# Kernel optimization log

Measured on AMD Instinct MI355X. Metric: run time of the kernel, lower is better.

Reference implementation:

```python
import jax, jax.numpy as jnp
import numpy as np

E = 768   # embed_size
H = 64    # head_embed_size
B = 8
T = 4096  # == ctx_size


def setup_inputs() -> dict:
    key = jax.random.key(0)
    k1, k2, k3, k4 = jax.random.split(key, 4)
    inputs = jax.random.normal(k1, (B, T, E), dtype=jnp.float32)
    # Linear weights stored as (E, H) so projection is x @ W
    scale = 1.0 / np.sqrt(E)
    Wq = jax.random.uniform(k2, (E, H), dtype=jnp.float32, minval=-scale, maxval=scale)
    Wk = jax.random.uniform(k3, (E, H), dtype=jnp.float32, minval=-scale, maxval=scale)
    Wv = jax.random.uniform(k4, (E, H), dtype=jnp.float32, minval=-scale, maxval=scale)
    return {"inputs": inputs, "Wq": Wq, "Wk": Wk, "Wv": Wv}


def reference(inputs, Wq, Wk, Wv):
    Tlen = inputs.shape[1]
    q = inputs @ Wq  # (B,T,H)
    k = inputs @ Wk  # (B,T,H)
    v = inputs @ Wv  # (B,T,H)
    # NOTE: original module does NOT scale by 1/sqrt(H) — faithful reproduction.
    scores = jnp.einsum('bqh,bkh->bqk', q, k)  # (B,T,T)
    causal = jnp.tril(jnp.ones((Tlen, Tlen), dtype=bool))
    scores = jnp.where(causal, scores, -jnp.inf)
    attn = jax.nn.softmax(scores, axis=-1)
    # dropout=0 -> identity
    out = jnp.einsum('bqk,bkh->bqh', attn, v)  # (B,T,H)
    return out
```

## Files before the change

### kernel.cpp

```cpp
#include <hip/hip_runtime.h>
#include <hip/hip_bf16.h>

#define E_DIM 768
#define H_DIM 64
#define B_SZ 8
#define T_SZ 4096
#define BT (B_SZ * T_SZ)

typedef __attribute__((ext_vector_type(8))) short short8;
typedef __attribute__((ext_vector_type(4))) float floatx4;

#define RAWBAR() __asm__ volatile("s_waitcnt lgkmcnt(0)\n\ts_barrier" ::: "memory")

static __device__ __forceinline__ unsigned short bf1(float a) {
    __hip_bfloat16 h = __float2bfloat16(a);
    unsigned short u; __builtin_memcpy(&u, &h, 2); return u;
}
static __device__ __forceinline__ unsigned int pk2(float a, float b) {
    __hip_bfloat162 h = __float22bfloat162_rn(float2{a, b});
    unsigned int u; __builtin_memcpy(&u, &h, 4); return u;
}

__global__ __launch_bounds__(256) void prep_w(
    const float* __restrict__ Wq, const float* __restrict__ Wk,
    const float* __restrict__ Wv, unsigned short* __restrict__ Wt)
{
    __shared__ float Ls[64][65];
    const int nt = blockIdx.x;
    const int kc = blockIdx.y;
    const float* __restrict__ W = (nt == 0) ? Wq : (nt == 1) ? Wk : Wv;
    const int t = threadIdx.x;
    const int k0 = kc * 64;

#pragma unroll
    for (int it = 0; it < 16; ++it) {
        const int kk = (t >> 6) + it * 4;
        Ls[kk][t & 63] = W[(size_t)(k0 + kk) * H_DIM + (t & 63)];
    }
    __syncthreads();

#pragma unroll
    for (int it = 0; it < 4; ++it) {
        const int nl = (t >> 4) + it * 16;
        const int kl = (t & 15) * 4;
        unsigned int u[2];
        u[0] = pk2(Ls[kl + 0][nl], Ls[kl + 1][nl]);
        u[1] = pk2(Ls[kl + 2][nl], Ls[kl + 3][nl]);
        *(uint2*)(Wt + (size_t)(nt * 64 + nl) * E_DIM + k0 + kl) = *(uint2*)u;
    }
}

__global__ __launch_bounds__(768) void proj_mfma(
    const float* __restrict__ X, const unsigned short* __restrict__ Wt,
    unsigned short* __restrict__ Qb, unsigned short* __restrict__ Kb,
    unsigned short* __restrict__ Vtb)
{
    __shared__ unsigned short Xs[2][16][776];

    const int tid  = threadIdx.x;
    const int wave = tid >> 6, lane = tid & 63;
    const int row  = lane & 15, quad = lane >> 4;
    const int m0   = blockIdx.x * 128;

    short8 bfr[24];
    {
        const unsigned short* wp = Wt + (size_t)(wave * 16 + row) * E_DIM + quad * 8;
#pragma unroll
        for (int ks = 0; ks < 24; ++ks) bfr[ks] = *(const short8*)(wp + ks * 32);
    }

    const int srow = tid & 15;
    const int sc   = tid >> 4;
    const float* __restrict__ xbase = X + (size_t)(m0 + srow) * E_DIM + sc * 16;

    float4 fx[4];
#define LDX(mt)                                                               \
    {                                                                         \
        const float* p = xbase + (size_t)(mt) * 16 * E_DIM;                   \
        fx[0] = *(const float4*)(p);     fx[1] = *(const float4*)(p + 4);     \
        fx[2] = *(const float4*)(p + 8); fx[3] = *(const float4*)(p + 12);    \
    }
#define STX(buf)                                                              \
    {                                                                         \
        unsigned int tmp[8];                                                  \
        tmp[0] = pk2(fx[0].x, fx[0].y); tmp[1] = pk2(fx[0].z, fx[0].w);       \
        tmp[2] = pk2(fx[1].x, fx[1].y); tmp[3] = pk2(fx[1].z, fx[1].w);       \
        tmp[4] = pk2(fx[2].x, fx[2].y); tmp[5] = pk2(fx[2].z, fx[2].w);       \
        tmp[6] = pk2(fx[3].x, fx[3].y); tmp[7] = pk2(fx[3].z, fx[3].w);       \
        *(int4*)&Xs[buf][srow][sc * 16]     = *(int4*)&tmp[0];                \
        *(int4*)&Xs[buf][srow][sc * 16 + 8] = *(int4*)&tmp[4];                \
    }

    LDX(0); STX(0);
    RAWBAR();

    const int g  = wave >> 2;
    const int h  = (wave & 3) * 16 + row;
    unsigned short* __restrict__ OQK = (g == 0) ? Qb : Kb;
    const int bb = m0 >> 12;

    int cur = 0;
    for (int mt = 0; mt < 8; ++mt) {
        if (mt < 7) LDX(mt + 1);

        floatx4 acc = (floatx4)0.0f;
#pragma unroll
        for (int ks = 0; ks < 24; ++ks) {
            const short8 af = *(const short8*)&Xs[cur][row][ks * 32 + quad * 8];
            acc = __builtin_amdgcn_mfma_f32_16x16x32_bf16(af, bfr[ks], acc, 0, 0, 0);
        }

        const int mr = m0 + mt * 16 + quad * 4;
        if (g < 2) {
#pragma unroll
            for (int r = 0; r < 4; ++r)
                OQK[(size_t)(mr + r) * H_DIM + h] = bf1(acc[r]);
        } else {
            const int t0 = mr & 4095;
            unsigned int u[2];
            u[0] = pk2(acc[0], acc[1]); u[1] = pk2(acc[2], acc[3]);
            *(uint2*)(Vtb + ((size_t)bb * H_DIM + h) * T_SZ + t0) = *(uint2*)u;
        }

        if (mt < 7) STX(cur ^ 1);
        RAWBAR();
        cur ^= 1;
    }
#undef LDX
#undef STX
}

typedef unsigned short KVrow[72];

__global__ __launch_bounds__(256) void attn_mfma(
    const unsigned short* __restrict__ Qb,
    const unsigned short* __restrict__ Kb,
    const unsigned short* __restrict__ Vtb,
    float* __restrict__ Out)
{
    __shared__ unsigned short Ks[3][64][72];
    __shared__ unsigned short Vs[3][64][72];
    __shared__ unsigned short Ps[4][16][76];

    const int lb   = blockIdx.x;
    const int b    = lb & 7;
    const int qt   = 63 - (lb >> 3);
    const int tid  = threadIdx.x;
    const int wave = tid >> 6, lane = tid & 63;
    const int row  = lane & 15, quad = lane >> 4;

    const size_t base = (size_t)b * T_SZ * H_DIM;
    const int q0 = qt * 64 + wave * 16;

    const int krow = tid >> 2, kcol = (tid & 3) * 16;
    const unsigned short* __restrict__ Ksrc = Kb + base + (size_t)krow * H_DIM + kcol;
    const int vh = tid >> 2, vseg = (tid & 3) * 16;
    const unsigned short* __restrict__ Vsrc = Vtb + ((size_t)b * H_DIM + vh) * T_SZ + vseg;

    short8 qf0, qf1;
    {
        const unsigned short* qp = Qb + base + (size_t)(q0 + row) * H_DIM + quad * 8;
        qf0 = *(const short8*)(qp);
        qf1 = *(const short8*)(qp + 32);
    }

    floatx4 o[4];
#pragma unroll
    for (int i = 0; i < 4; ++i) o[i] = (floatx4)0.0f;
    float lp[4] = {0.0f, 0.0f, 0.0f, 0.0f};

    KVrow* kp0 = Ks[0]; KVrow* kp1 = Ks[1]; KVrow* kp2 = Ks[2];
    KVrow* vp0 = Vs[0]; KVrow* vp1 = Vs[1]; KVrow* vp2 = Vs[2];

    int4 kA0, kA1, vA0, vA1, kB0, kB1, vB0, vB1;

#define LDKV(K0, K1, V0, V1, t)                                          \
    {                                                                    \
        const unsigned short* kp = Ksrc + (size_t)(t) * 64 * H_DIM;      \
        K0 = *(const int4*)kp; K1 = *(const int4*)(kp + 8);              \
        const unsigned short* vp = Vsrc + (t) * 64;                      \
        V0 = *(const int4*)vp; V1 = *(const int4*)(vp + 8);              \
    }
#define STKV(K0, K1, V0, V1, KD, VD)                                     \
    {                                                                    \
        *(int4*)&KD[krow][kcol] = K0; *(int4*)&KD[krow][kcol + 8] = K1;  \
        *(int4*)&VD[vh][vseg]   = V0; *(int4*)&VD[vh][vseg + 8]   = V1;  \
    }
#define ROTATE()                                                         \
    { KVrow* tk = kp0; kp0 = kp1; kp1 = kp2; kp2 = tk;                   \
      KVrow* tv = vp0; vp0 = vp1; vp1 = vp2; vp2 = tv; }

    auto compute = [&](int t, KVrow* kc, KVrow* vc) {
        floatx4 s[4];
#pragma unroll
        for (int nt = 0; nt < 4; ++nt) {
            const unsigned short* kp = &kc[nt * 16 + row][quad * 8];
            floatx4 a = (floatx4)0.0f;
            a = __builtin_amdgcn_mfma_f32_16x16x32_bf16(qf0, *(const short8*)(kp),      a, 0, 0, 0);
            a = __builtin_amdgcn_mfma_f32_16x16x32_bf16(qf1, *(const short8*)(kp + 32), a, 0, 0, 0);
            s[nt] = a;
        }
        if (t == qt) {
#pragma unroll
            for (int nt = 0; nt < 4; ++nt) {
                const int key_loc = nt * 16 + row;
#pragma unroll
                for (int r = 0; r < 4; ++r)
                    if (key_loc > wave * 16 + quad * 4 + r) s[nt][r] = -1e30f;
            }
        }
#pragma unroll
        for (int r = 0; r < 4; ++r) {
#pragma unroll
            for (int nt = 0; nt < 4; ++nt) {
                const float pv = __expf(fminf(s[nt][r], 80.0f));
                lp[r] += pv;
                Ps[wave][quad * 4 + r][nt * 16 + row] = bf1(pv);
            }
        }
        __builtin_amdgcn_wave_barrier();
#pragma unroll
        for (int kst = 0; kst < 2; ++kst) {
            const short8 pa = *(const short8*)(&Ps[wave][row][kst * 32 + quad * 8]);
#pragma unroll
            for (int nt = 0; nt < 4; ++nt) {
                const short8 vb = *(const short8*)(&vc[nt * 16 + row][kst * 32 + quad * 8]);
                o[nt] = __builtin_amdgcn_mfma_f32_16x16x32_bf16(pa, vb, o[nt], 0, 0, 0);
            }
        }
    };

    LDKV(kA0, kA1, vA0, vA1, 0);
    STKV(kA0, kA1, vA0, vA1, kp0, vp0);
    if (qt >= 1) LDKV(kB0, kB1, vB0, vB1, 1);
    RAWBAR();

    int kt = 0;
    while (true) {
        if (kt + 2 <= qt) LDKV(kA0, kA1, vA0, vA1, kt + 2);
        if (kt + 1 <= qt) STKV(kB0, kB1, vB0, vB1, kp1, vp1);
        compute(kt, kp0, vp0);
        RAWBAR();
        ROTATE();
        ++kt;
        if (kt > qt) break;

        if (kt + 2 <= qt) LDKV(kB0, kB1, vB0, vB1, kt + 2);
        if (kt + 1 <= qt) STKV(kA0, kA1, vA0, vA1, kp1, vp1);
        compute(kt, kp0, vp0);
        RAWBAR();
        ROTATE();
        ++kt;
        if (kt > qt) break;
    }

#pragma unroll
    for (int r = 0; r < 4; ++r) {
        float l = lp[r];
#pragma unroll
        for (int off = 1; off < 16; off <<= 1)
            l += __shfl_xor(l, off, 16);
        const float inv = 1.0f / l;
        float* op = Out + base + (size_t)(q0 + quad * 4 + r) * H_DIM + row;
#pragma unroll
        for (int nt = 0; nt < 4; ++nt)
            op[nt * 16] = o[nt][r] * inv;
    }
#undef LDKV
#undef STKV
#undef ROTATE
}

extern "C" void kernel_launch(void* const* d_in, const int* in_sizes, int n_in,
                              void* d_out, int out_size, void* d_ws, size_t ws_size,
                              hipStream_t stream) {
    const float* X  = (const float*)d_in[0];
    const float* Wq = (const float*)d_in[1];
    const float* Wk = (const float*)d_in[2];
    const float* Wv = (const float*)d_in[3];

    unsigned short* Wt  = (unsigned short*)d_ws;
    unsigned short* Qb  = Wt + (size_t)192 * E_DIM;
    unsigned short* Kb  = Qb + (size_t)BT * H_DIM;
    unsigned short* Vtb = Kb + (size_t)BT * H_DIM;

    prep_w<<<dim3(3, 12), 256, 0, stream>>>(Wq, Wk, Wv, Wt);
    proj_mfma<<<256, 768, 0, stream>>>(X, Wt, Qb, Kb, Vtb);
    attn_mfma<<<512, 256, 0, stream>>>(Qb, Kb, Vtb, (float*)d_out);
}
```

Measured before the change: 237.9 us.

## Split attention key range across waves with 16-row query blocks and LDS reduction

The attention kernel now assigns 16 query rows per block and splits the causal key tiles across the four waves, which load K and V fragments straight from global memory into registers instead of staging them in shared memory. Partial outputs and row sums are combined through LDS at the end, and the grid grows from 512 to 2048 blocks. The scale log2(e) is folded into Wq so the softmax can use exp2f, removing a multiply per score. This drops the block-wide barriers and the LDS staging, and gives finer causal load balance. In exchange, global/L2 traffic per block rises, and each wave's K/V loads are less coalesced.

Measured after the change: 291.1 us. 1.22x slower.

```diff
diff --git a/kernel.cpp b/kernel.cpp
--- a/kernel.cpp
+++ b/kernel.cpp
@@ -29,6 +29,7 @@
     const int nt = blockIdx.x;
     const int kc = blockIdx.y;
     const float* __restrict__ W = (nt == 0) ? Wq : (nt == 1) ? Wk : Wv;
+    const float scl = (nt == 0) ? 1.44269504088896f : 1.0f;
     const int t = threadIdx.x;
     const int k0 = kc * 64;
 
@@ -44,8 +45,8 @@
         const int nl = (t >> 4) + it * 16;
         const int kl = (t & 15) * 4;
         unsigned int u[2];
-        u[0] = pk2(Ls[kl + 0][nl], Ls[kl + 1][nl]);
-        u[1] = pk2(Ls[kl + 2][nl], Ls[kl + 3][nl]);
+        u[0] = pk2(Ls[kl + 0][nl] * scl, Ls[kl + 1][nl] * scl);
+        u[1] = pk2(Ls[kl + 2][nl] * scl, Ls[kl + 3][nl] * scl);
         *(uint2*)(Wt + (size_t)(nt * 64 + nl) * E_DIM + k0 + kl) = *(uint2*)u;
     }
 }
@@ -130,36 +131,31 @@
 #undef STX
 }
 
-typedef unsigned short KVrow[72];
-
-__global__ __launch_bounds__(256) void attn_mfma(
+__global__ __launch_bounds__(256, 3) void attn_mfma(
     const unsigned short* __restrict__ Qb,
     const unsigned short* __restrict__ Kb,
     const unsigned short* __restrict__ Vtb,
     float* __restrict__ Out)
 {
-    __shared__ unsigned short Ks[3][64][72];
-    __shared__ unsigned short Vs[3][64][72];
     __shared__ unsigned short Ps[4][16][76];
+    __shared__ float Oc[4][16][64];
+    __shared__ float lc[4][16];
 
     const int lb   = blockIdx.x;
     const int b    = lb & 7;
-    const int qt   = 63 - (lb >> 3);
+    const int qq   = 255 - (lb >> 3);
     const int tid  = threadIdx.x;
     const int wave = tid >> 6, lane = tid & 63;
-    const int row  = lane & 15, quad = lane >> 4;
+    const int col  = lane & 15, quad = lane >> 4;
 
     const size_t base = (size_t)b * T_SZ * H_DIM;
-    const int q0 = qt * 64 + wave * 16;
-
-    const int krow = tid >> 2, kcol = (tid & 3) * 16;
-    const unsigned short* __restrict__ Ksrc = Kb + base + (size_t)krow * H_DIM + kcol;
-    const int vh = tid >> 2, vseg = (tid & 3) * 16;
-    const unsigned short* __restrict__ Vsrc = Vtb + ((size_t)b * H_DIM + vh) * T_SZ + vseg;
+    const int q0  = qq * 16;
+    const int nkt = (qq >> 2) + 1;
+    const int ktd = nkt - 1;
 
     short8 qf0, qf1;
     {
-        const unsigned short* qp = Qb + base + (size_t)(q0 + row) * H_DIM + quad * 8;
+        const unsigned short* qp = Qb + base + (size_t)(q0 + col) * H_DIM + quad * 8;
         qf0 = *(const short8*)(qp);
         qf1 = *(const short8*)(qp + 32);
     }
@@ -169,89 +165,79 @@
     for (int i = 0; i < 4; ++i) o[i] = (floatx4)0.0f;
     float lp[4] = {0.0f, 0.0f, 0.0f, 0.0f};
 
-    KVrow* kp0 = Ks[0]; KVrow* kp1 = Ks[1]; KVrow* kp2 = Ks[2];
-    KVrow* vp0 = Vs[0]; KVrow* vp1 = Vs[1]; KVrow* vp2 = Vs[2];
-
-    int4 kA0, kA1, vA0, vA1, kB0, kB1, vB0, vB1;
-
-#define LDKV(K0, K1, V0, V1, t)                                          \
-    {                                                                    \
-        const unsigned short* kp = Ksrc + (size_t)(t) * 64 * H_DIM;      \
-        K0 = *(const int4*)kp; K1 = *(const int4*)(kp + 8);              \
-        const unsigned short* vp = Vsrc + (t) * 64;                      \
-        V0 = *(const int4*)vp; V1 = *(const int4*)(vp + 8);              \
-    }
-#define STKV(K0, K1, V0, V1, KD, VD)                                     \
-    {                                                                    \
-        *(int4*)&KD[krow][kcol] = K0; *(int4*)&KD[krow][kcol + 8] = K1;  \
-        *(int4*)&VD[vh][vseg]   = V0; *(int4*)&VD[vh][vseg + 8]   = V1;  \
-    }
-#define ROTATE()                                                         \
-    { KVrow* tk = kp0; kp0 = kp1; kp1 = kp2; kp2 = tk;                   \
-      KVrow* tv = vp0; vp0 = vp1; vp1 = vp2; vp2 = tv; }
-
-    auto compute = [&](int t, KVrow* kc, KVrow* vc) {
+    const unsigned short* __restrict__ Kfb = Kb + base + (size_t)col * H_DIM + quad * 8;
+    const unsigned short* __restrict__ Vfb = Vtb + ((size_t)b * H_DIM + col) * T_SZ + quad * 8;
+
+    short8 kA[8], kB[8];
+
+#define LOADK(dst, kt)                                                        \
+    {                                                                         \
+        const unsigned short* kp = Kfb + (size_t)(kt) * 64 * H_DIM;           \
+        _Pragma("unroll")                                                     \
+        for (int nt = 0; nt < 4; ++nt) {                                      \
+            dst[nt * 2 + 0] = *(const short8*)(kp + nt * 16 * H_DIM);         \
+            dst[nt * 2 + 1] = *(const short8*)(kp + nt * 16 * H_DIM + 32);    \
+        }                                                                     \
+    }
+
+    auto compute = [&](int kt, const short8 (&kf)[8]) {
+        short8 vf[8];
+#pragma unroll
+        for (int nt = 0; nt < 4; ++nt) {
+            const unsigned short* vp = Vfb + (size_t)nt * 16 * T_SZ + kt * 64;
+            vf[nt * 2 + 0] = *(const short8*)(vp);
+            vf[nt * 2 + 1] = *(const short8*)(vp + 32);
+        }
+
         floatx4 s[4];
 #pragma unroll
         for (int nt = 0; nt < 4; ++nt) {
-            const unsigned short* kp = &kc[nt * 16 + row][quad * 8];
             floatx4 a = (floatx4)0.0f;
-            a = __builtin_amdgcn_mfma_f32_16x16x32_bf16(qf0, *(const short8*)(kp),      a, 0, 0, 0);
-            a = __builtin_amdgcn_mfma_f32_16x16x32_bf16(qf1, *(const short8*)(kp + 32), a, 0, 0, 0);
+            a = __builtin_amdgcn_mfma_f32_16x16x32_bf16(qf0, kf[nt * 2 + 0], a, 0, 0, 0);
+            a = __builtin_amdgcn_mfma_f32_16x16x32_bf16(qf1, kf[nt * 2 + 1], a, 0, 0, 0);
             s[nt] = a;
         }
-        if (t == qt) {
+
+        if (kt == ktd) {
 #pragma unroll
             for (int nt = 0; nt < 4; ++nt) {
-                const int key_loc = nt * 16 + row;
+                const int keyg = kt * 64 + nt * 16 + col;
 #pragma unroll
                 for (int r = 0; r < 4; ++r)
-                    if (key_loc > wave * 16 + quad * 4 + r) s[nt][r] = -1e30f;
+                    if (keyg > q0 + quad * 4 + r) s[nt][r] = -1e30f;
             }
         }
+
 #pragma unroll
         for (int r = 0; r < 4; ++r) {
 #pragma unroll
             for (int nt = 0; nt < 4; ++nt) {
-                const float pv = __expf(fminf(s[nt][r], 80.0f));
+                const float pv = exp2f(fminf(s[nt][r], 110.0f));
                 lp[r] += pv;
-                Ps[wave][quad * 4 + r][nt * 16 + row] = bf1(pv);
+                Ps[wave][quad * 4 + r][nt * 16 + col] = bf1(pv);
             }
         }
         __builtin_amdgcn_wave_barrier();
-#pragma unroll
-        for (int kst = 0; kst < 2; ++kst) {
-            const short8 pa = *(const short8*)(&Ps[wave][row][kst * 32 + quad * 8]);
-#pragma unroll
-            for (int nt = 0; nt < 4; ++nt) {
-                const short8 vb = *(const short8*)(&vc[nt * 16 + row][kst * 32 + quad * 8]);
-                o[nt] = __builtin_amdgcn_mfma_f32_16x16x32_bf16(pa, vb, o[nt], 0, 0, 0);
-            }
+
+#pragma unroll
+        for (int ks = 0; ks < 2; ++ks) {
+            const short8 pa = *(const short8*)(&Ps[wave][col][ks * 32 + quad * 8]);
+#pragma unroll
+            for (int nt = 0; nt < 4; ++nt)
+                o[nt] = __builtin_amdgcn_mfma_f32_16x16x32_bf16(pa, vf[nt * 2 + ks], o[nt], 0, 0, 0);
         }
     };
 
-    LDKV(kA0, kA1, vA0, vA1, 0);
-    STKV(kA0, kA1, vA0, vA1, kp0, vp0);
-    if (qt >= 1) LDKV(kB0, kB1, vB0, vB1, 1);
-    RAWBAR();
-
-    int kt = 0;
-    while (true) {
-        if (kt + 2 <= qt) LDKV(kA0, kA1, vA0, vA1, kt + 2);
-        if (kt + 1 <= qt) STKV(kB0, kB1, vB0, vB1, kp1, vp1);
-        compute(kt, kp0, vp0);
-        RAWBAR();
-        ROTATE();
-        ++kt;
-        if (kt > qt) break;
-
-        if (kt + 2 <= qt) LDKV(kB0, kB1, vB0, vB1, kt + 2);
-        if (kt + 1 <= qt) STKV(kA0, kA1, vA0, vA1, kp1, vp1);
-        compute(kt, kp0, vp0);
-        RAWBAR();
-        ROTATE();
-        ++kt;
-        if (kt > qt) break;
+    int kt = wave;
+    if (kt < nkt) LOADK(kA, kt);
+    while (kt < nkt) {
+        if (kt + 4 < nkt) LOADK(kB, kt + 4);
+        compute(kt, kA);
+        kt += 4;
+        if (kt >= nkt) break;
+        if (kt + 4 < nkt) LOADK(kA, kt + 4);
+        compute(kt, kB);
+        kt += 4;
     }
 
 #pragma unroll
@@ -260,15 +246,27 @@
 #pragma unroll
         for (int off = 1; off < 16; off <<= 1)
             l += __shfl_xor(l, off, 16);
+        if (col == 0) lc[wave][quad * 4 + r] = l;
+#pragma unroll
+        for (int nt = 0; nt < 4; ++nt)
+            Oc[wave][quad * 4 + r][nt * 16 + col] = o[nt][r];
+    }
+    __syncthreads();
+
+    {
+        const int orow = tid >> 4, d0 = (tid & 15) * 4;
+        float4 acc = {0.0f, 0.0f, 0.0f, 0.0f};
+#pragma unroll
+        for (int w = 0; w < 4; ++w) {
+            const float4 t4 = *(const float4*)&Oc[w][orow][d0];
+            acc.x += t4.x; acc.y += t4.y; acc.z += t4.z; acc.w += t4.w;
+        }
+        const float l = lc[0][orow] + lc[1][orow] + lc[2][orow] + lc[3][orow];
         const float inv = 1.0f / l;
-        float* op = Out + base + (size_t)(q0 + quad * 4 + r) * H_DIM + row;
-#pragma unroll
-        for (int nt = 0; nt < 4; ++nt)
-            op[nt * 16] = o[nt][r] * inv;
-    }
-#undef LDKV
-#undef STKV
-#undef ROTATE
+        acc.x *= inv; acc.y *= inv; acc.z *= inv; acc.w *= inv;
+        *(float4*)(Out + base + (size_t)(q0 + orow) * H_DIM + d0) = acc;
+    }
+#undef LOADK
 }
 
 extern "C" void kernel_launch(void* const* d_in, const int* in_sizes, int n_in,
@@ -286,5 +284,5 @@
 
     prep_w<<<dim3(3, 12), 256, 0, stream>>>(Wq, Wk, Wv, Wt);
     proj_mfma<<<256, 768, 0, stream>>>(X, Wt, Qb, Kb, Vtb);
-    attn_mfma<<<512, 256, 0, stream>>>(Qb, Kb, Vtb, (float*)d_out);
-}
+    attn_mfma<<<2048, 256, 0, stream>>>(Qb, Kb, Vtb, (float*)d_out);
+}
```

## Split attention into 32-query blocks with key-split waves and exp2 prescaling

Applied to the files above, without the earlier changes.

The attention kernel now uses 32-query tiles with 1024 blocks. Four waves form a 2x2 grid over query rows and key halves, and the two key-split partial outputs and row sums are combined through shared memory before a vectorized float4 store. Wq is prescaled by log2(e) during weight prep so softmax can use exp2f. The K/V pipeline drops from a triple to a single shared buffer with register prefetch, and launch bounds request 4 blocks per CU. The goal is better load balance and occupancy on the causal triangle. The cost is an extra barrier per tile, less load-store overlap, and a cross-wave reduction epilogue.

Result: faster. 230.8 us (-3.0%).

```diff
diff --git a/kernel.cpp b/kernel.cpp
--- a/kernel.cpp
+++ b/kernel.cpp
@@ -29,6 +29,7 @@
     const int nt = blockIdx.x;
     const int kc = blockIdx.y;
     const float* __restrict__ W = (nt == 0) ? Wq : (nt == 1) ? Wk : Wv;
+    const float scl = (nt == 0) ? 1.44269504088896f : 1.0f;
     const int t = threadIdx.x;
     const int k0 = kc * 64;
 
@@ -44,8 +45,8 @@
         const int nl = (t >> 4) + it * 16;
         const int kl = (t & 15) * 4;
         unsigned int u[2];
-        u[0] = pk2(Ls[kl + 0][nl], Ls[kl + 1][nl]);
-        u[1] = pk2(Ls[kl + 2][nl], Ls[kl + 3][nl]);
+        u[0] = pk2(Ls[kl + 0][nl] * scl, Ls[kl + 1][nl] * scl);
+        u[1] = pk2(Ls[kl + 2][nl] * scl, Ls[kl + 3][nl] * scl);
         *(uint2*)(Wt + (size_t)(nt * 64 + nl) * E_DIM + k0 + kl) = *(uint2*)u;
     }
 }
@@ -130,128 +131,110 @@
 #undef STX
 }
 
-typedef unsigned short KVrow[72];
-
-__global__ __launch_bounds__(256) void attn_mfma(
+__global__ __launch_bounds__(256, 4) void attn_mfma(
     const unsigned short* __restrict__ Qb,
     const unsigned short* __restrict__ Kb,
     const unsigned short* __restrict__ Vtb,
     float* __restrict__ Out)
 {
-    __shared__ unsigned short Ks[3][64][72];
-    __shared__ unsigned short Vs[3][64][72];
-    __shared__ unsigned short Ps[4][16][76];
+    __shared__ __align__(16) unsigned short KV[2][64][72];
+    __shared__ __align__(16) unsigned short Ps[4][16][40];
+    __shared__ float lc[4][16];
 
     const int lb   = blockIdx.x;
     const int b    = lb & 7;
-    const int qt   = 63 - (lb >> 3);
+    const int qq   = 127 - (lb >> 3);
     const int tid  = threadIdx.x;
     const int wave = tid >> 6, lane = tid & 63;
-    const int row  = lane & 15, quad = lane >> 4;
+    const int col  = lane & 15, quad = lane >> 4;
+    const int wq   = wave >> 1;
+    const int wk   = wave & 1;
 
     const size_t base = (size_t)b * T_SZ * H_DIM;
-    const int q0 = qt * 64 + wave * 16;
+    const int q0  = qq * 32;
+    const int nkt = (qq >> 1) + 1;
+    const int ktd = nkt - 1;
+
+    short8 qf0, qf1;
+    {
+        const unsigned short* qp = Qb + base + (size_t)(q0 + wq * 16 + col) * H_DIM + quad * 8;
+        qf0 = *(const short8*)(qp);
+        qf1 = *(const short8*)(qp + 32);
+    }
+
+    floatx4 o[4];
+#pragma unroll
+    for (int i = 0; i < 4; ++i) o[i] = (floatx4)0.0f;
+    float lp[4] = {0.0f, 0.0f, 0.0f, 0.0f};
 
     const int krow = tid >> 2, kcol = (tid & 3) * 16;
     const unsigned short* __restrict__ Ksrc = Kb + base + (size_t)krow * H_DIM + kcol;
-    const int vh = tid >> 2, vseg = (tid & 3) * 16;
-    const unsigned short* __restrict__ Vsrc = Vtb + ((size_t)b * H_DIM + vh) * T_SZ + vseg;
-
-    short8 qf0, qf1;
-    {
-        const unsigned short* qp = Qb + base + (size_t)(q0 + row) * H_DIM + quad * 8;
-        qf0 = *(const short8*)(qp);
-        qf1 = *(const short8*)(qp + 32);
-    }
-
-    floatx4 o[4];
-#pragma unroll
-    for (int i = 0; i < 4; ++i) o[i] = (floatx4)0.0f;
-    float lp[4] = {0.0f, 0.0f, 0.0f, 0.0f};
-
-    KVrow* kp0 = Ks[0]; KVrow* kp1 = Ks[1]; KVrow* kp2 = Ks[2];
-    KVrow* vp0 = Vs[0]; KVrow* vp1 = Vs[1]; KVrow* vp2 = Vs[2];
-
-    int4 kA0, kA1, vA0, vA1, kB0, kB1, vB0, vB1;
-
-#define LDKV(K0, K1, V0, V1, t)                                          \
+    const unsigned short* __restrict__ Vsrc = Vtb + ((size_t)b * H_DIM + krow) * T_SZ + kcol;
+
+    int4 kr0, kr1, vr0, vr1;
+#define LDKV(t)                                                          \
     {                                                                    \
         const unsigned short* kp = Ksrc + (size_t)(t) * 64 * H_DIM;      \
-        K0 = *(const int4*)kp; K1 = *(const int4*)(kp + 8);              \
+        kr0 = *(const int4*)kp; kr1 = *(const int4*)(kp + 8);            \
         const unsigned short* vp = Vsrc + (t) * 64;                      \
-        V0 = *(const int4*)vp; V1 = *(const int4*)(vp + 8);              \
-    }
-#define STKV(K0, K1, V0, V1, KD, VD)                                     \
+        vr0 = *(const int4*)vp; vr1 = *(const int4*)(vp + 8);            \
+    }
+#define STKV()                                                           \
     {                                                                    \
-        *(int4*)&KD[krow][kcol] = K0; *(int4*)&KD[krow][kcol + 8] = K1;  \
-        *(int4*)&VD[vh][vseg]   = V0; *(int4*)&VD[vh][vseg + 8]   = V1;  \
-    }
-#define ROTATE()                                                         \
-    { KVrow* tk = kp0; kp0 = kp1; kp1 = kp2; kp2 = tk;                   \
-      KVrow* tv = vp0; vp0 = vp1; vp1 = vp2; vp2 = tv; }
-
-    auto compute = [&](int t, KVrow* kc, KVrow* vc) {
-        floatx4 s[4];
-#pragma unroll
-        for (int nt = 0; nt < 4; ++nt) {
-            const unsigned short* kp = &kc[nt * 16 + row][quad * 8];
+        *(int4*)&KV[0][krow][kcol] = kr0; *(int4*)&KV[0][krow][kcol + 8] = kr1; \
+        *(int4*)&KV[1][krow][kcol] = vr0; *(int4*)&KV[1][krow][kcol + 8] = vr1; \
+    }
+
+    LDKV(0);
+    STKV();
+    RAWBAR();
+
+    for (int kt = 0; kt < nkt; ++kt) {
+        if (kt + 1 < nkt) LDKV(kt + 1);
+
+        floatx4 s[2];
+#pragma unroll
+        for (int j = 0; j < 2; ++j) {
+            const unsigned short* kp = &KV[0][(wk * 2 + j) * 16 + col][quad * 8];
             floatx4 a = (floatx4)0.0f;
             a = __builtin_amdgcn_mfma_f32_16x16x32_bf16(qf0, *(const short8*)(kp),      a, 0, 0, 0);
             a = __builtin_amdgcn_mfma_f32_16x16x32_bf16(qf1, *(const short8*)(kp + 32), a, 0, 0, 0);
-            s[nt] = a;
-        }
-        if (t == qt) {
-#pragma unroll
-            for (int nt = 0; nt < 4; ++nt) {
-                const int key_loc = nt * 16 + row;
+            s[j] = a;
+        }
+
+        if (kt == ktd) {
+#pragma unroll
+            for (int j = 0; j < 2; ++j) {
+                const int keyg = kt * 64 + wk * 32 + j * 16 + col;
 #pragma unroll
                 for (int r = 0; r < 4; ++r)
-                    if (key_loc > wave * 16 + quad * 4 + r) s[nt][r] = -1e30f;
+                    if (keyg > q0 + wq * 16 + quad * 4 + r) s[j][r] = -1e30f;
             }
         }
+
 #pragma unroll
         for (int r = 0; r < 4; ++r) {
 #pragma unroll
-            for (int nt = 0; nt < 4; ++nt) {
-                const float pv = __expf(fminf(s[nt][r], 80.0f));
+            for (int j = 0; j < 2; ++j) {
+                const float pv = exp2f(fminf(s[j][r], 110.0f));
                 lp[r] += pv;
-                Ps[wave][quad * 4 + r][nt * 16 + row] = bf1(pv);
+                Ps[wave][quad * 4 + r][j * 16 + col] = bf1(pv);
             }
         }
         __builtin_amdgcn_wave_barrier();
-#pragma unroll
-        for (int kst = 0; kst < 2; ++kst) {
-            const short8 pa = *(const short8*)(&Ps[wave][row][kst * 32 + quad * 8]);
-#pragma unroll
-            for (int nt = 0; nt < 4; ++nt) {
-                const short8 vb = *(const short8*)(&vc[nt * 16 + row][kst * 32 + quad * 8]);
-                o[nt] = __builtin_amdgcn_mfma_f32_16x16x32_bf16(pa, vb, o[nt], 0, 0, 0);
+
+        {
+            const short8 pa = *(const short8*)(&Ps[wave][col][quad * 8]);
+#pragma unroll
+            for (int d = 0; d < 4; ++d) {
+                const short8 vb = *(const short8*)(&KV[1][d * 16 + col][wk * 32 + quad * 8]);
+                o[d] = __builtin_amdgcn_mfma_f32_16x16x32_bf16(pa, vb, o[d], 0, 0, 0);
             }
         }
-    };
-
-    LDKV(kA0, kA1, vA0, vA1, 0);
-    STKV(kA0, kA1, vA0, vA1, kp0, vp0);
-    if (qt >= 1) LDKV(kB0, kB1, vB0, vB1, 1);
-    RAWBAR();
-
-    int kt = 0;
-    while (true) {
-        if (kt + 2 <= qt) LDKV(kA0, kA1, vA0, vA1, kt + 2);
-        if (kt + 1 <= qt) STKV(kB0, kB1, vB0, vB1, kp1, vp1);
-        compute(kt, kp0, vp0);
+
         RAWBAR();
-        ROTATE();
-        ++kt;
-        if (kt > qt) break;
-
-        if (kt + 2 <= qt) LDKV(kB0, kB1, vB0, vB1, kt + 2);
-        if (kt + 1 <= qt) STKV(kA0, kA1, vA0, vA1, kp1, vp1);
-        compute(kt, kp0, vp0);
+        if (kt + 1 < nkt) STKV();
         RAWBAR();
-        ROTATE();
-        ++kt;
-        if (kt > qt) break;
     }
 
 #pragma unroll
@@ -260,15 +243,40 @@
 #pragma unroll
         for (int off = 1; off < 16; off <<= 1)
             l += __shfl_xor(l, off, 16);
-        const float inv = 1.0f / l;
-        float* op = Out + base + (size_t)(q0 + quad * 4 + r) * H_DIM + row;
-#pragma unroll
-        for (int nt = 0; nt < 4; ++nt)
-            op[nt * 16] = o[nt][r] * inv;
+        if (col == 0) lc[wave][quad * 4 + r] = l;
+    }
+    __syncthreads();
+
+    float* __restrict__ Oc = (float*)&KV[0][0][0];
+#pragma unroll
+    for (int r = 0; r < 4; ++r)
+#pragma unroll
+        for (int d = 0; d < 4; ++d)
+            Oc[((wave * 16) + quad * 4 + r) * 64 + d * 16 + col] = o[d][r];
+    __syncthreads();
+
+    {
+        const int orow = tid >> 3;
+        const int d0   = (tid & 7) * 8;
+        const int rl   = orow & 15;
+        const int wb   = (orow >> 4) * 2;
+        const float* p0 = &Oc[((wb * 16) + rl) * 64 + d0];
+        const float* p1 = &Oc[(((wb + 1) * 16) + rl) * 64 + d0];
+        const float inv = 1.0f / (lc[wb][rl] + lc[wb + 1][rl]);
+        float4 a0 = *(const float4*)(p0);
+        float4 a1 = *(const float4*)(p0 + 4);
+        const float4 b0 = *(const float4*)(p1);
+        const float4 b1 = *(const float4*)(p1 + 4);
+        a0.x = (a0.x + b0.x) * inv; a0.y = (a0.y + b0.y) * inv;
+        a0.z = (a0.z + b0.z) * inv; a0.w = (a0.w + b0.w) * inv;
+        a1.x = (a1.x + b1.x) * inv; a1.y = (a1.y + b1.y) * inv;
+        a1.z = (a1.z + b1.z) * inv; a1.w = (a1.w + b1.w) * inv;
+        float* op = Out + base + (size_t)(q0 + orow) * H_DIM + d0;
+        *(float4*)(op)     = a0;
+        *(float4*)(op + 4) = a1;
     }
 #undef LDKV
 #undef STKV
-#undef ROTATE
 }
 
 extern "C" void kernel_launch(void* const* d_in, const int* in_sizes, int n_in,
@@ -286,5 +294,5 @@
 
     prep_w<<<dim3(3, 12), 256, 0, stream>>>(Wq, Wk, Wv, Wt);
     proj_mfma<<<256, 768, 0, stream>>>(X, Wt, Qb, Kb, Vtb);
-    attn_mfma<<<512, 256, 0, stream>>>(Qb, Kb, Vtb, (float*)d_out);
-}
+    attn_mfma<<<1024, 256, 0, stream>>>(Qb, Kb, Vtb, (float*)d_out);
+}
```
